# Kernel optimization log

Hardware: AMD Instinct MI355X
Metric: run time of the kernel (lower is better)

## Reference

```python
import jax, jax.numpy as jnp
import numpy as np

EMB = 1024
HEADS = 8
NUM_REL = 5
BS = 8
SLEN = 1024


def setup_inputs() -> dict:
    key = jax.random.key(0)
    ks = jax.random.split(key, 11)

    def lin(k, out_dim, in_dim):
        k1, k2 = jax.random.split(k)
        w = 0.02 * jax.random.normal(k1, (out_dim, in_dim), dtype=jnp.float32)
        b = 0.02 * jax.random.normal(k2, (out_dim,), dtype=jnp.float32)
        return w, b

    p = {}
    for i, pref in enumerate(["nq", "nk", "nv", "no", "tq", "tk", "tv", "to"]):
        w, b = lin(ks[i], EMB, EMB)
        p[pref + "_w"] = w
        p[pref + "_b"] = b
    tp_w, tp_b = lin(ks[8], NUM_REL, EMB)
    h_in = jax.random.normal(ks[9], (BS, SLEN, EMB), dtype=jnp.float32)
    word_mask = jnp.ones((BS, SLEN), dtype=bool)
    return {"h_in": h_in, "word_mask": word_mask, **p, "tp_w": tp_w, "tp_b": tp_b}


def _mha(x, mask, qw, qb, kw, kb, vw, vb, ow, ob):
    # Self-attention with key-padding mask; returns (output, attn_weights).
    bs, slen, dim = x.shape
    dh = dim // HEADS

    def split(t):  # [bs, slen, dim] -> [bs, h, slen, dh]
        return t.reshape(bs, slen, HEADS, dh).transpose(0, 2, 1, 3)

    q = split(x @ qw.T + qb) / jnp.sqrt(jnp.asarray(dh, x.dtype))
    k = split(x @ kw.T + kb)
    v = split(x @ vw.T + vb)
    scores = jnp.einsum('bhqd,bhkd->bhqk', q, k)
    scores = jnp.where(mask[:, None, None, :], scores, jnp.asarray(-1e9, x.dtype))
    w = jax.nn.softmax(scores, axis=-1)  # [bs, h, slen, slen]
    ctx = jnp.einsum('bhqk,bhkd->bhqd', w, v).transpose(0, 2, 1, 3).reshape(bs, slen, dim)
    return ctx @ ow.T + ob, w


def reference(h_in, word_mask, nq_w, nq_b, nk_w, nk_b, nv_w, nv_b, no_w, no_b,
              tq_w, tq_b, tk_w, tk_b, tv_w, tv_b, to_w, to_b, tp_w, tp_b):
    # Edge norms: sum attention weights over heads, then symmetrize.
    _, norm_w = _mha(h_in, word_mask, nq_w, nq_b, nk_w, nk_b, nv_w, nv_b, no_w, no_b)
    norm_w = norm_w.sum(axis=1)  # edge_norm_agg == 'sum' -> [bs, slen, slen]
    norms = norm_w + norm_w.transpose(0, 2, 1)

    # Edge types: second attention, project to relation logits, pairwise outer-sum.
    type_out, _ = _mha(h_in, word_mask, tq_w, tq_b, tk_w, tk_b, tv_w, tv_b, to_w, to_b)
    logits = type_out @ tp_w.T + tp_b  # [bs, slen, R]
    pair = logits[:, :, None, :] + logits[:, None, :, :]  # [bs, slen, slen, R]
    type_probs = jax.nn.softmax(pair, axis=-1)  # log_softmax(...).exp()
    return norms, type_probs
```

## Files before the change

### kernel.cpp

```cpp
#include <hip/hip_runtime.h>

using u16 = unsigned short;
typedef __bf16 bf16x8 __attribute__((ext_vector_type(8)));
typedef float  f32x4  __attribute__((ext_vector_type(4)));

__device__ __forceinline__ float b2f(u16 u){
  union { unsigned int i; float f; } v; v.i = ((unsigned int)u) << 16; return v.f;
}
__device__ __forceinline__ u16 f2b(float f){
  union { float f; unsigned int i; } v; v.f = f;
  unsigned int r = v.i + 0x7FFFu + ((v.i >> 16) & 1u);
  return (u16)(r >> 16);
}
__device__ __forceinline__ float waveMax(float v){
  #pragma unroll
  for (int o = 32; o > 0; o >>= 1) v = fmaxf(v, __shfl_xor(v, o, 64));
  return v;
}
__device__ __forceinline__ float waveSum(float v){
  #pragma unroll
  for (int o = 32; o > 0; o >>= 1) v += __shfl_xor(v, o, 64);
  return v;
}
__device__ __forceinline__ void async_cp16(const u16* g, u16* l){
  __builtin_amdgcn_global_load_lds((const __attribute__((address_space(1))) void*)g,
                                   (__attribute__((address_space(3))) void*)l, 16, 0, 0);
}

__global__ __launch_bounds__(256)
void cvt_f2b4(const float* __restrict__ s, u16* __restrict__ d, long long n4)
{
  long long i = (long long)blockIdx.x * 256 + threadIdx.x;
  long long st = (long long)gridDim.x * 256;
  for (; i < n4; i += st) {
    float4 v = ((const float4*)s)[i];
    ushort4 o; o.x = f2b(v.x); o.y = f2b(v.y); o.z = f2b(v.z); o.w = f2b(v.w);
    ((ushort4*)d)[i] = o;
  }
}

__global__ __launch_bounds__(256)
void bcat_k(const float* b0, const float* b1, const float* b2, const float* b3,
            const float* b4, float* __restrict__ dst)
{
  int t = blockIdx.x * 256 + threadIdx.x;
  const float* s = (t < 1024) ? b0 : (t < 2048) ? b1 : (t < 3072) ? b2 : (t < 4096) ? b3 : b4;
  dst[t] = s[t & 1023];
}

__global__ __launch_bounds__(256)
void fuse_w(const float* __restrict__ tow, const float* __restrict__ tob,
            const float* __restrict__ tpw, const float* __restrict__ tpb,
            float* __restrict__ Wc, float* __restrict__ bc)
{
  int t = blockIdx.x * 256 + threadIdx.x;
  int r = t >> 10, c = t & 1023;
  float acc = 0.f;
  for (int k = 0; k < 1024; k++) acc += tpw[r * 1024 + k] * tow[k * 1024 + c];
  Wc[t] = acc;
  if (t < 5) {
    float a = 0.f;
    for (int k = 0; k < 1024; k++) a += tpw[t * 1024 + k] * tob[k];
    bc[t] = a + tpb[t];
  }
}

template<int HAS_BIAS>
__global__ __launch_bounds__(256)
void gemm_bt(const u16* __restrict__ A, const u16* __restrict__ B,
             u16* __restrict__ C, const float* __restrict__ bias,
             int lda, int ldb, int ldc, int K,
             long long sAo, long long sAi, long long sBo, long long sBi,
             long long sCo, long long sCi, int zshift, int zmask, float alpha)
{
  int zo = (int)(blockIdx.z >> zshift), zi = (int)(blockIdx.z & zmask);
  A += zo * sAo + zi * sAi;
  B += zo * sBo + zi * sBi;
  long long coff = zo * sCo + zi * sCi;
  int m0 = blockIdx.y * 128, n0 = blockIdx.x * 128;

  __shared__ alignas(16) u16 sA[128 * 32];
  __shared__ alignas(16) u16 sB[128 * 32];

  int t = threadIdx.x;
  int lane = t & 63, wave = t >> 6;
  int quad = lane >> 4, l16 = lane & 15;
  int wm = (wave >> 1) << 6, wn = (wave & 1) << 6;
  int srow = t >> 2, scg = (t & 3) << 3;
  int wb = wave << 9;

  const u16* ga = A + (long long)(m0 + srow) * lda + scg;
  const u16* gb = B + (long long)(n0 + srow) * ldb + scg;

  f32x4 acc[4][4] = {};

  for (int k0 = 0; k0 < K; k0 += 32) {
    __syncthreads();
    async_cp16(ga + k0,                sA + wb);
    async_cp16(ga + 64ll * lda + k0,   sA + wb + 2048);
    async_cp16(gb + k0,                sB + wb);
    async_cp16(gb + 64ll * ldb + k0,   sB + wb + 2048);
    __syncthreads();

    bf16x8 af[4], bfr[4];
    #pragma unroll
    for (int mi = 0; mi < 4; mi++)
      af[mi] = *(const bf16x8*)(&sA[(wm + mi * 16 + l16) * 32 + quad * 8]);
    #pragma unroll
    for (int ni = 0; ni < 4; ni++)
      bfr[ni] = *(const bf16x8*)(&sB[(wn + ni * 16 + l16) * 32 + quad * 8]);
    #pragma unroll
    for (int mi = 0; mi < 4; mi++)
      #pragma unroll
      for (int ni = 0; ni < 4; ni++)
        acc[mi][ni] = __builtin_amdgcn_mfma_f32_16x16x32_bf16(af[mi], bfr[ni], acc[mi][ni], 0, 0, 0);
  }

  #pragma unroll
  for (int ni = 0; ni < 4; ni++) {
    int n = n0 + wn + ni * 16 + l16;
    float bv = 0.f;
    if (HAS_BIAS) bv = bias[n];
    #pragma unroll
    for (int mi = 0; mi < 4; mi++) {
      int mb = m0 + wm + mi * 16 + quad * 4;
      #pragma unroll
      for (int r = 0; r < 4; r++) {
        float v = alpha * (acc[mi][ni][r] + bv);
        C[coff + (long long)(mb + r) * ldc + n] = f2b(v);
      }
    }
  }
}

__global__ __launch_bounds__(256)
void transpose_v(const u16* __restrict__ src, u16* __restrict__ vT)
{
  int jt = blockIdx.x, dt = blockIdx.y, bh = blockIdx.z;
  int b = bh >> 3, h = bh & 7;
  __shared__ u16 s[64][65];
  int t = threadIdx.x;
  #pragma unroll
  for (int p = 0; p < 16; p++) {
    int idx = p * 256 + t; int jj = idx >> 6, dd = idx & 63;
    s[jj][dd] = src[(long long)(b * 1024 + jt * 64 + jj) * 5120 + 4096 + h * 128 + dt * 64 + dd];
  }
  __syncthreads();
  #pragma unroll
  for (int p = 0; p < 16; p++) {
    int idx = p * 256 + t; int dd = idx >> 6, jj = idx & 63;
    vT[((long long)bh * 128 + dt * 64 + dd) * 1024 + jt * 64 + jj] = s[jj][dd];
  }
}

__global__ __launch_bounds__(256)
void norm_softmax_sum(const u16* __restrict__ sc, float* __restrict__ out)
{
  int i = blockIdx.x, b = blockIdx.y;
  int t = threadIdx.x;
  int wave = t >> 6;
  __shared__ float wm_[4], wsu[4];
  float acc[4] = {0.f, 0.f, 0.f, 0.f};

  for (int h = 0; h < 8; h++) {
    const u16* row = sc + (((long long)(b * 8 + h)) << 20) + ((long long)i << 10);
    float v[4];
    #pragma unroll
    for (int p = 0; p < 4; p++) v[p] = b2f(row[t + 256 * p]);
    float m = fmaxf(fmaxf(v[0], v[1]), fmaxf(v[2], v[3]));
    m = waveMax(m);
    if ((t & 63) == 0) wm_[wave] = m;
    __syncthreads();
    m = fmaxf(fmaxf(wm_[0], wm_[1]), fmaxf(wm_[2], wm_[3]));
    float e[4], s = 0.f;
    #pragma unroll
    for (int p = 0; p < 4; p++) { e[p] = __expf(v[p] - m); s += e[p]; }
    s = waveSum(s);
    if ((t & 63) == 0) wsu[wave] = s;
    __syncthreads();
    s = wsu[0] + wsu[1] + wsu[2] + wsu[3];
    float inv = 1.f / s;
    #pragma unroll
    for (int p = 0; p < 4; p++) acc[p] += e[p] * inv;
  }
  float* o = out + ((long long)b << 20) + ((long long)i << 10);
  #pragma unroll
  for (int p = 0; p < 4; p++) o[t + 256 * p] = acc[p];
}

__global__ __launch_bounds__(256)
void type_softmax(u16* __restrict__ sc)
{
  u16* row = sc + (((long long)blockIdx.y) << 20) + ((long long)blockIdx.x << 10);
  int t = threadIdx.x;
  int wave = t >> 6;
  __shared__ float wm_[4], wsu[4];
  float v[4];
  #pragma unroll
  for (int p = 0; p < 4; p++) v[p] = b2f(row[t + 256 * p]);
  float m = fmaxf(fmaxf(v[0], v[1]), fmaxf(v[2], v[3]));
  m = waveMax(m);
  if ((t & 63) == 0) wm_[wave] = m;
  __syncthreads();
  m = fmaxf(fmaxf(wm_[0], wm_[1]), fmaxf(wm_[2], wm_[3]));
  float e[4], s = 0.f;
  #pragma unroll
  for (int p = 0; p < 4; p++) { e[p] = __expf(v[p] - m); s += e[p]; }
  s = waveSum(s);
  if ((t & 63) == 0) wsu[wave] = s;
  __syncthreads();
  s = wsu[0] + wsu[1] + wsu[2] + wsu[3];
  float inv = 1.f / s;
  #pragma unroll
  for (int p = 0; p < 4; p++) row[t + 256 * p] = f2b(e[p] * inv);
}

__global__ __launch_bounds__(256)
void sym_inplace(float* __restrict__ nw)
{
  int tj = blockIdx.x, ti = blockIdx.y, b = blockIdx.z;
  if (tj < ti) return;
  float* base = nw + ((long long)b << 20);
  __shared__ float sij[64][65], sji[64][65];
  int t = threadIdx.x;
  #pragma unroll
  for (int p = 0; p < 16; p++) {
    int idx = p * 256 + t; int r = idx >> 6, c = idx & 63;
    sij[r][c] = base[(long long)(ti * 64 + r) * 1024 + tj * 64 + c];
    sji[r][c] = base[(long long)(tj * 64 + r) * 1024 + ti * 64 + c];
  }
  __syncthreads();
  #pragma unroll
  for (int p = 0; p < 16; p++) {
    int idx = p * 256 + t; int r = idx >> 6, c = idx & 63;
    base[(long long)(ti * 64 + r) * 1024 + tj * 64 + c] = sij[r][c] + sji[c][r];
    if (ti != tj)
      base[(long long)(tj * 64 + r) * 1024 + ti * 64 + c] = sji[r][c] + sij[c][r];
  }
}

__global__ __launch_bounds__(256)
void logits_k(const u16* __restrict__ ctx, const float* __restrict__ Wc,
              const float* __restrict__ bc, float* __restrict__ lg)
{
  int wave = threadIdx.x >> 6, l = threadIdx.x & 63;
  int row = blockIdx.x * 4 + wave;
  const u16* cr = ctx + (long long)row * 1024;
  bf16x8 v0 = ((const bf16x8*)cr)[l * 2];
  bf16x8 v1 = ((const bf16x8*)cr)[l * 2 + 1];
  float x[16];
  #pragma unroll
  for (int j = 0; j < 8; j++) { x[j] = (float)v0[j]; x[8 + j] = (float)v1[j]; }
  float p[5];
  #pragma unroll
  for (int r = 0; r < 5; r++) {
    float a = 0.f;
    const float* wr = Wc + r * 1024 + l * 16;
    #pragma unroll
    for (int j = 0; j < 16; j++) a += x[j] * wr[j];
    p[r] = waveSum(a);
  }
  if (l == 0) {
    #pragma unroll
    for (int r = 0; r < 5; r++) lg[(long long)row * 5 + r] = p[r] + bc[r];
  }
}

__global__ __launch_bounds__(256)
void pairwise_probs(const float* __restrict__ lg, float* __restrict__ out)
{
  int i = blockIdx.x, b = blockIdx.y;
  int t = threadIdx.x;
  __shared__ float sin_[5120];
  __shared__ float sout[5120];
  const float* lb = lg + (long long)b * 5120;
  #pragma unroll
  for (int p = 0; p < 20; p++) sin_[p * 256 + t] = lb[p * 256 + t];
  __syncthreads();
  float li[5];
  #pragma unroll
  for (int r = 0; r < 5; r++) li[r] = sin_[i * 5 + r];
  #pragma unroll
  for (int p = 0; p < 4; p++) {
    int j = t + 256 * p;
    float x[5]; float m = -1e30f;
    #pragma unroll
    for (int r = 0; r < 5; r++) { x[r] = li[r] + sin_[j * 5 + r]; m = fmaxf(m, x[r]); }
    float s = 0.f;
    #pragma unroll
    for (int r = 0; r < 5; r++) { x[r] = __expf(x[r] - m); s += x[r]; }
    float inv = 1.f / s;
    #pragma unroll
    for (int r = 0; r < 5; r++) sout[j * 5 + r] = x[r] * inv;
  }
  __syncthreads();
  float4* ob = (float4*)(out + ((long long)(b * 1024 + i)) * 5120);
  #pragma unroll
  for (int q = 0; q < 5; q++) ob[q * 256 + t] = ((const float4*)sout)[q * 256 + t];
}

extern "C" void kernel_launch(void* const* d_in, const int* in_sizes, int n_in,
                              void* d_out, int out_size, void* d_ws, size_t ws_size,
                              hipStream_t stream)
{
  const float* h_in = (const float*)d_in[0];
  const float* nq_w = (const float*)d_in[2];
  const float* nq_b = (const float*)d_in[3];
  const float* nk_w = (const float*)d_in[4];
  const float* nk_b = (const float*)d_in[5];
  const float* tq_w = (const float*)d_in[10];
  const float* tq_b = (const float*)d_in[11];
  const float* tk_w = (const float*)d_in[12];
  const float* tk_b = (const float*)d_in[13];
  const float* tv_w = (const float*)d_in[14];
  const float* tv_b = (const float*)d_in[15];
  const float* to_w = (const float*)d_in[16];
  const float* to_b = (const float*)d_in[17];
  const float* tp_w = (const float*)d_in[18];
  const float* tp_b = (const float*)d_in[19];

  char* ws = (char*)d_ws;
  u16*  hb   = (u16*)(ws);
  u16*  wcat = (u16*)(ws + (16ll  << 20));
  float* bcat= (float*)(ws + (26ll << 20));
  float* Wc  = (float*)(ws + (26ll << 20) + (512 << 10));
  float* bc  = (float*)(ws + (26ll << 20) + (768 << 10));
  float* lg  = (float*)(ws + (27ll << 20));
  u16*  proj = (u16*)(ws + (28ll  << 20));
  u16*  vT   = (u16*)(ws + (108ll << 20));
  u16*  ctx  = (u16*)(ws + (124ll << 20));
  u16*  sc   = (u16*)(ws + (140ll << 20));

  float* out_norms = (float*)d_out;
  float* out_types = (float*)d_out + 8388608ll;

  const float qs = 0.08838834764831845f;
  dim3 blk(256);

  cvt_f2b4<<<dim3(2048), blk, 0, stream>>>(h_in, hb, 2097152ll);
  cvt_f2b4<<<dim3(512),  blk, 0, stream>>>(nq_w, wcat,              262144ll);
  cvt_f2b4<<<dim3(512),  blk, 0, stream>>>(nk_w, wcat + 1048576ll,  262144ll);
  cvt_f2b4<<<dim3(512),  blk, 0, stream>>>(tq_w, wcat + 2097152ll,  262144ll);
  cvt_f2b4<<<dim3(512),  blk, 0, stream>>>(tk_w, wcat + 3145728ll,  262144ll);
  cvt_f2b4<<<dim3(512),  blk, 0, stream>>>(tv_w, wcat + 4194304ll,  262144ll);
  bcat_k<<<dim3(20), blk, 0, stream>>>(nq_b, nk_b, tq_b, tk_b, tv_b, bcat);
  fuse_w<<<dim3(20), blk, 0, stream>>>(to_w, to_b, tp_w, tp_b, Wc, bc);

  gemm_bt<1><<<dim3(40,64,1), blk, 0, stream>>>(hb, wcat, proj, bcat,
      1024,1024,5120,1024, 0,0,0,0,0,0, 0,0, 1.f);
  transpose_v<<<dim3(16,2,64), blk, 0, stream>>>(proj, vT);

  gemm_bt<0><<<dim3(8,8,64), blk, 0, stream>>>(proj, proj + 1024, sc, nullptr,
      5120,5120,1024,128, 5242880ll,128ll, 5242880ll,128ll, 8388608ll,1048576ll, 3,7, qs);
  norm_softmax_sum<<<dim3(1024,8), blk, 0, stream>>>(sc, out_norms);
  sym_inplace<<<dim3(16,16,8), blk, 0, stream>>>(out_norms);

  gemm_bt<0><<<dim3(8,8,64), blk, 0, stream>>>(proj + 2048, proj + 3072, sc, nullptr,
      5120,5120,1024,128, 5242880ll,128ll, 5242880ll,128ll, 8388608ll,1048576ll, 3,7, qs);
  type_softmax<<<dim3(1024,64), blk, 0, stream>>>(sc);
  gemm_bt<0><<<dim3(1,8,64), blk, 0, stream>>>(sc, vT, ctx, nullptr,
      1024,1024,1024,1024, 8388608ll,1048576ll, 1048576ll,131072ll, 1048576ll,128ll, 3,7, 1.f);
  logits_k<<<dim3(2048), blk, 0, stream>>>(ctx, Wc, bc, lg);
  pairwise_probs<<<dim3(1024,8), blk, 0, stream>>>(lg, out_types);
}
```

Measured before the change: 805.5 us.

## Fold output and relation projections into V before softmax-weighted sum

Uses associativity to project each head's V rows onto the five fused relation weights first (w5 = V_h·Wc_h), so the type-attention context GEMM, the V transpose and the separate logits kernel are no longer needed. A new fused kernel computes each row's softmax and immediately reduces it against w5, summing over heads to produce the logits directly. This removes a full write and reread of the softmax probabilities and a large PV GEMM. The trade-off is a scalar reduction path in place of matrix-core MFMA and different bf16 rounding points.

```diff
diff --git a/kernel.cpp b/kernel.cpp
--- a/kernel.cpp
+++ b/kernel.cpp
@@ -134,26 +134,6 @@
 }
 
 __global__ __launch_bounds__(256)
-void transpose_v(const u16* __restrict__ src, u16* __restrict__ vT)
-{
-  int jt = blockIdx.x, dt = blockIdx.y, bh = blockIdx.z;
-  int b = bh >> 3, h = bh & 7;
-  __shared__ u16 s[64][65];
-  int t = threadIdx.x;
-  #pragma unroll
-  for (int p = 0; p < 16; p++) {
-    int idx = p * 256 + t; int jj = idx >> 6, dd = idx & 63;
-    s[jj][dd] = src[(long long)(b * 1024 + jt * 64 + jj) * 5120 + 4096 + h * 128 + dt * 64 + dd];
-  }
-  __syncthreads();
-  #pragma unroll
-  for (int p = 0; p < 16; p++) {
-    int idx = p * 256 + t; int dd = idx >> 6, jj = idx & 63;
-    vT[((long long)bh * 128 + dt * 64 + dd) * 1024 + jt * 64 + jj] = s[jj][dd];
-  }
-}
-
-__global__ __launch_bounds__(256)
 void norm_softmax_sum(const u16* __restrict__ sc, float* __restrict__ out)
 {
   int i = blockIdx.x, b = blockIdx.y;
@@ -186,33 +166,6 @@
   float* o = out + ((long long)b << 20) + ((long long)i << 10);
   #pragma unroll
   for (int p = 0; p < 4; p++) o[t + 256 * p] = acc[p];
-}
-
-__global__ __launch_bounds__(256)
-void type_softmax(u16* __restrict__ sc)
-{
-  u16* row = sc + (((long long)blockIdx.y) << 20) + ((long long)blockIdx.x << 10);
-  int t = threadIdx.x;
-  int wave = t >> 6;
-  __shared__ float wm_[4], wsu[4];
-  float v[4];
-  #pragma unroll
-  for (int p = 0; p < 4; p++) v[p] = b2f(row[t + 256 * p]);
-  float m = fmaxf(fmaxf(v[0], v[1]), fmaxf(v[2], v[3]));
-  m = waveMax(m);
-  if ((t & 63) == 0) wm_[wave] = m;
-  __syncthreads();
-  m = fmaxf(fmaxf(wm_[0], wm_[1]), fmaxf(wm_[2], wm_[3]));
-  float e[4], s = 0.f;
-  #pragma unroll
-  for (int p = 0; p < 4; p++) { e[p] = __expf(v[p] - m); s += e[p]; }
-  s = waveSum(s);
-  if ((t & 63) == 0) wsu[wave] = s;
-  __syncthreads();
-  s = wsu[0] + wsu[1] + wsu[2] + wsu[3];
-  float inv = 1.f / s;
-  #pragma unroll
-  for (int p = 0; p < 4; p++) row[t + 256 * p] = f2b(e[p] * inv);
 }
 
 __global__ __launch_bounds__(256)
@@ -240,29 +193,78 @@
 }
 
 __global__ __launch_bounds__(256)
-void logits_k(const u16* __restrict__ ctx, const float* __restrict__ Wc,
-              const float* __restrict__ bc, float* __restrict__ lg)
-{
-  int wave = threadIdx.x >> 6, l = threadIdx.x & 63;
-  int row = blockIdx.x * 4 + wave;
-  const u16* cr = ctx + (long long)row * 1024;
-  bf16x8 v0 = ((const bf16x8*)cr)[l * 2];
-  bf16x8 v1 = ((const bf16x8*)cr)[l * 2 + 1];
-  float x[16];
-  #pragma unroll
-  for (int j = 0; j < 8; j++) { x[j] = (float)v0[j]; x[8 + j] = (float)v1[j]; }
-  float p[5];
-  #pragma unroll
-  for (int r = 0; r < 5; r++) {
-    float a = 0.f;
-    const float* wr = Wc + r * 1024 + l * 16;
-    #pragma unroll
-    for (int j = 0; j < 16; j++) a += x[j] * wr[j];
-    p[r] = waveSum(a);
-  }
+void w5_k(const u16* __restrict__ proj, const float* __restrict__ Wc,
+          float* __restrict__ w5)
+{
+  int jb = blockIdx.x, bh = blockIdx.y;
+  int b = bh >> 3, h = bh & 7;
+  int t = threadIdx.x;
+  int j = jb * 256 + t;
+  __shared__ float sWc[5][128];
+  if (t < 128) {
+    #pragma unroll
+    for (int r = 0; r < 5; r++) sWc[r][t] = Wc[r * 1024 + h * 128 + t];
+  }
+  __syncthreads();
+  const u16* vrow = proj + (long long)(b * 1024 + j) * 5120 + 4096 + h * 128;
+  float acc[5] = {0.f, 0.f, 0.f, 0.f, 0.f};
+  #pragma unroll
+  for (int d0 = 0; d0 < 128; d0 += 8) {
+    bf16x8 v = *(const bf16x8*)(vrow + d0);
+    #pragma unroll
+    for (int q = 0; q < 8; q++) {
+      float f = (float)v[q];
+      #pragma unroll
+      for (int r = 0; r < 5; r++) acc[r] += f * sWc[r][d0 + q];
+    }
+  }
+  #pragma unroll
+  for (int r = 0; r < 5; r++) w5[(((long long)(bh * 5 + r)) << 10) + j] = acc[r];
+}
+
+__global__ __launch_bounds__(256)
+void type_logits(const u16* __restrict__ sc, const float* __restrict__ w5,
+                 const float* __restrict__ bc, float* __restrict__ lg)
+{
+  int b = blockIdx.y;
+  int t = threadIdx.x;
+  int wave = t >> 6, l = t & 63;
+  int i = blockIdx.x * 4 + wave;
+  __shared__ float sW5[5120];
+  float acc[5] = {0.f, 0.f, 0.f, 0.f, 0.f};
+
+  for (int h = 0; h < 8; h++) {
+    const u16* row = sc + (((long long)(b * 8 + h)) << 20) + ((long long)i << 10);
+    const float* wb = w5 + ((long long)(b * 8 + h)) * 5120;
+    float v[16];
+    #pragma unroll
+    for (int k = 0; k < 16; k++) v[k] = b2f(row[l + 64 * k]);
+    __syncthreads();
+    #pragma unroll
+    for (int p = 0; p < 20; p++) sW5[p * 256 + t] = wb[p * 256 + t];
+    float m = v[0];
+    #pragma unroll
+    for (int k = 1; k < 16; k++) m = fmaxf(m, v[k]);
+    m = waveMax(m);
+    float e[16], s = 0.f;
+    #pragma unroll
+    for (int k = 0; k < 16; k++) { e[k] = __expf(v[k] - m); s += e[k]; }
+    s = waveSum(s);
+    float inv = 1.f / s;
+    __syncthreads();
+    #pragma unroll
+    for (int r = 0; r < 5; r++) {
+      float a = 0.f;
+      #pragma unroll
+      for (int k = 0; k < 16; k++) a += e[k] * sW5[r * 1024 + l + 64 * k];
+      acc[r] += a * inv;
+    }
+  }
+  #pragma unroll
+  for (int r = 0; r < 5; r++) acc[r] = waveSum(acc[r]);
   if (l == 0) {
     #pragma unroll
-    for (int r = 0; r < 5; r++) lg[(long long)row * 5 + r] = p[r] + bc[r];
+    for (int r = 0; r < 5; r++) lg[(long long)(b * 1024 + i) * 5 + r] = acc[r] + bc[r];
   }
 }
 
@@ -327,8 +329,7 @@
   float* bc  = (float*)(ws + (26ll << 20) + (768 << 10));
   float* lg  = (float*)(ws + (27ll << 20));
   u16*  proj = (u16*)(ws + (28ll  << 20));
-  u16*  vT   = (u16*)(ws + (108ll << 20));
-  u16*  ctx  = (u16*)(ws + (124ll << 20));
+  float* w5  = (float*)(ws + (108ll << 20));
   u16*  sc   = (u16*)(ws + (140ll << 20));
 
   float* out_norms = (float*)d_out;
@@ -348,7 +349,8 @@
 
   gemm_bt<1><<<dim3(40,64,1), blk, 0, stream>>>(hb, wcat, proj, bcat,
       1024,1024,5120,1024, 0,0,0,0,0,0, 0,0, 1.f);
-  transpose_v<<<dim3(16,2,64), blk, 0, stream>>>(proj, vT);
+
+  w5_k<<<dim3(4,64), blk, 0, stream>>>(proj, Wc, w5);
 
   gemm_bt<0><<<dim3(8,8,64), blk, 0, stream>>>(proj, proj + 1024, sc, nullptr,
       5120,5120,1024,128, 5242880ll,128ll, 5242880ll,128ll, 8388608ll,1048576ll, 3,7, qs);
@@ -357,9 +359,6 @@
 
   gemm_bt<0><<<dim3(8,8,64), blk, 0, stream>>>(proj + 2048, proj + 3072, sc, nullptr,
       5120,5120,1024,128, 5242880ll,128ll, 5242880ll,128ll, 8388608ll,1048576ll, 3,7, qs);
-  type_softmax<<<dim3(1024,64), blk, 0, stream>>>(sc);
-  gemm_bt<0><<<dim3(1,8,64), blk, 0, stream>>>(sc, vT, ctx, nullptr,
-      1024,1024,1024,1024, 8388608ll,1048576ll, 1048576ll,131072ll, 1048576ll,128ll, 3,7, 1.f);
-  logits_k<<<dim3(2048), blk, 0, stream>>>(ctx, Wc, bc, lg);
+  type_logits<<<dim3(256,8), blk, 0, stream>>>(sc, w5, bc, lg);
   pairwise_probs<<<dim3(1024,8), blk, 0, stream>>>(lg, out_types);
 }
```

Result: faster. 741.8 us (-7.9%).
